# Optimization experiments

Hardware: AMD Instinct MI355X
Metric: run time of the kernel (lower is better)

Reference implementation:

```python
import jax, jax.numpy as jnp
import numpy as np

NUM_HEADS = 16
SQ, B, E = 2048, 4, 1024
SKV = 2049  # 1 text token + SQ motion tokens


def setup_inputs() -> dict:
    key = jax.random.key(0)
    ks = jax.random.split(key, 12)
    s = 1.0 / np.sqrt(E)
    inp = {
        "q": jax.random.normal(ks[0], (SQ, B, E), jnp.float32),
        "kv": jax.random.normal(ks[1], (SKV, B, E), jnp.float32),
        "cond_positions_mask": jax.random.bernoulli(ks[2], 0.3, (B, SQ)),
        "Wq": jax.random.uniform(ks[3], (E, E), jnp.float32, -s, s),
        "bq": jnp.zeros((E,), jnp.float32),
        "Wk": jax.random.uniform(ks[4], (E, E), jnp.float32, -s, s),
        "bk": jnp.zeros((E,), jnp.float32),
        "Wv": jax.random.uniform(ks[5], (E, E), jnp.float32, -s, s),
        "bv": jnp.zeros((E,), jnp.float32),
        "Wo": jax.random.uniform(ks[6], (E, E), jnp.float32, -s, s),
        "bo": jnp.zeros((E,), jnp.float32),
    }
    return inp


def _dual_causal_mask(cond_positions_mask, seq_len_q, seq_len_kv):
    # returns (B, Sq, Skv) bool, True = masked out
    motion_len = seq_len_kv - 1
    i = jnp.arange(seq_len_q)[:, None]
    j = jnp.arange(motion_len)[None, :]
    causal = (i < j)[None]                                  # (1, Sq, ml)
    ci = cond_positions_mask[:, :, None]                    # (B, Sq, 1)
    cj = cond_positions_mask[:, None, :motion_len]          # (B, 1, ml)
    cond_to_cond = ci & cj
    cond_to_gen = ci & ~cj
    motion_mask = (causal & ~cond_to_cond) | cond_to_gen    # (B, Sq, ml)
    b = cond_positions_mask.shape[0]
    text_col = jnp.zeros((b, seq_len_q, 1), bool)           # text token always visible
    return jnp.concatenate([text_col, motion_mask], axis=-1)


def reference(q, kv, cond_positions_mask, Wq, bq, Wk, bk, Wv, bv, Wo, bo):
    seq_len_q, batch, embed_dim = q.shape
    seq_len_kv = kv.shape[0]
    head_dim = embed_dim // NUM_HEADS
    qb = q.transpose(1, 0, 2)   # (B, Sq, E)
    kvb = kv.transpose(1, 0, 2)  # (B, Skv, E)
    Q = (qb @ Wq.T + bq).reshape(batch, seq_len_q, NUM_HEADS, head_dim)
    K = (kvb @ Wk.T + bk).reshape(batch, seq_len_kv, NUM_HEADS, head_dim)
    V = (kvb @ Wv.T + bv).reshape(batch, seq_len_kv, NUM_HEADS, head_dim)
    scores = jnp.einsum("bqhd,bkhd->bhqk", Q, K) / np.sqrt(head_dim).astype(np.float32)
    mask = _dual_causal_mask(cond_positions_mask, seq_len_q, seq_len_kv)
    scores = jnp.where(mask[:, None], -jnp.inf, scores)
    attn = jax.nn.softmax(scores, axis=-1)                  # (B, H, Sq, Skv)
    out = jnp.einsum("bhqk,bkhd->bqhd", attn, V).reshape(batch, seq_len_q, embed_dim)
    out = out @ Wo.T + bo
    return out.transpose(1, 0, 2), attn.mean(axis=1)
```

## Files before the change

### kernel.cpp

```cpp
#include <hip/hip_runtime.h>
#include <hip/hip_bf16.h>

#define B_ 4
#define H_ 16
#define D_ 64
#define E_ 1024
#define SQ_ 2048
#define SKV_ 2049
#define SKVP_ 2080
#define QSCALE 0.18033688011112042f

typedef __attribute__((ext_vector_type(8))) short short8;
typedef __attribute__((ext_vector_type(4))) float f32x4;
typedef __attribute__((ext_vector_type(16))) float f32x16;
typedef __attribute__((ext_vector_type(4))) unsigned int u32x4;
typedef __attribute__((ext_vector_type(4))) float float4v;

static __device__ __forceinline__ float ex2(float x) {
    return __builtin_amdgcn_exp2f(x);
}

static __device__ __forceinline__ unsigned short f2bf(float f) {
    unsigned int u = __float_as_uint(f);
    u += 0x7FFFu + ((u >> 16) & 1u);
    return (unsigned short)(u >> 16);
}
static __device__ __forceinline__ unsigned int pack2(float a, float b) {
    union { __hip_bfloat162 h; unsigned int u; } cv;
    cv.h = __float22bfloat162_rn(make_float2(a, b));
    return cv.u;
}

static __device__ __forceinline__ f32x4 mfma16(short8 a, short8 b, f32x4 c) {
    return __builtin_amdgcn_mfma_f32_16x16x32_bf16(a, b, c, 0, 0, 0);
}
static __device__ __forceinline__ f32x16 mfma32(short8 a, short8 b, f32x16 c) {
    return __builtin_amdgcn_mfma_f32_32x32x16_bf16(a, b, c, 0, 0, 0);
}

__global__ void cvt_bf16_kernel(const float* __restrict__ in,
                                unsigned short* __restrict__ out, int n8) {
    for (int i = blockIdx.x * blockDim.x + threadIdx.x; i < n8; i += gridDim.x * blockDim.x) {
        const float4v a = *(const float4v*)&in[(size_t)i * 8];
        const float4v b = *(const float4v*)&in[(size_t)i * 8 + 4];
        u32x4 o;
        o[0] = pack2(a[0], a[1]);
        o[1] = pack2(a[2], a[3]);
        o[2] = pack2(b[0], b[1]);
        o[3] = pack2(b[2], b[3]);
        *(u32x4*)&out[(size_t)i * 8] = o;
    }
}

__global__ void decode_mask_kernel(const void* __restrict__ mraw,
                                   unsigned char* __restrict__ condm) {
    __shared__ int flags[2];
    const int t = threadIdx.x;
    if (t < 2) flags[t] = 1;
    __syncthreads();
    const unsigned int* wp = (const unsigned int*)mraw;
    int okI = 1, okF = 1;
    for (int i = t; i < 2048; i += 256) {
        unsigned int w = wp[i];
        if (w > 1u) okI = 0;
        if (w != 0u && w != 0x3F800000u) okF = 0;
    }
    if (!okI) atomicAnd(&flags[0], 0);
    if (!okF) atomicAnd(&flags[1], 0);
    __syncthreads();
    const int isWord = flags[0] | flags[1];
    for (int i = t; i < B_ * SQ_; i += 256) {
        unsigned char v;
        if (isWord) v = (unsigned char)(wp[i] != 0u);
        else        v = (unsigned char)(((const unsigned char*)mraw)[i] != 0);
        condm[i] = v;
    }
}

template <int MODE>
__global__ __launch_bounds__(256, 2)
void gemm128_kernel(const unsigned short* __restrict__ Abf,
                    const unsigned short* __restrict__ Wbf,
                    const float* __restrict__ bias, void* __restrict__ Outp,
                    int nrows, int nrb) {
    const int bid = blockIdx.x;
    const int xcd = bid & 7;
    const int pos = bid >> 3;
    const int cb = pos & 7;
    const int rb = (pos >> 3) * 8 + xcd;
    if (rb >= nrb) return;
    const int row0 = rb * 128, col0 = cb * 128;

    __shared__ unsigned short As[128][40];
    __shared__ unsigned short Ws[128][40];
    const int t = threadIdx.x;
    const int w = t >> 6, lane = t & 63;
    const int wm = w >> 1, wn = w & 1;
    const int lr = lane & 15, lg = lane >> 4, lk = lg * 8;
    const int srow = t >> 1, sc0 = (t & 1) * 16;
    int ar = row0 + srow;
    if (ar >= nrows) ar = nrows - 1;
    const int wrow = col0 + srow;

    f32x4 acc[4][4] = {};

#pragma unroll 1
    for (int k0 = 0; k0 < E_; k0 += 32) {
        {
            const unsigned short* ap = &Abf[(size_t)ar * E_ + k0 + sc0];
            *(short8*)&As[srow][sc0] = *(const short8*)&ap[0];
            *(short8*)&As[srow][sc0 + 8] = *(const short8*)&ap[8];
        }
        {
            const unsigned short* wp2 = &Wbf[(size_t)wrow * E_ + k0 + sc0];
            *(short8*)&Ws[srow][sc0] = *(const short8*)&wp2[0];
            *(short8*)&Ws[srow][sc0 + 8] = *(const short8*)&wp2[8];
        }
        __syncthreads();
        short8 af[4], bf[4];
#pragma unroll
        for (int mi = 0; mi < 4; ++mi) af[mi] = *(const short8*)&As[wm * 64 + mi * 16 + lr][lk];
#pragma unroll
        for (int ni = 0; ni < 4; ++ni) bf[ni] = *(const short8*)&Ws[wn * 64 + ni * 16 + lr][lk];
#pragma unroll
        for (int mi = 0; mi < 4; ++mi)
#pragma unroll
            for (int ni = 0; ni < 4; ++ni)
                acc[mi][ni] = mfma16(af[mi], bf[ni], acc[mi][ni]);
        __syncthreads();
    }

#pragma unroll
    for (int ni = 0; ni < 4; ++ni) {
        const int c = col0 + wn * 64 + ni * 16 + lr;
        const float bv = bias[c];
        const int h = c >> 6, d = c & 63;
#pragma unroll
        for (int mi = 0; mi < 4; ++mi) {
#pragma unroll
            for (int r4 = 0; r4 < 4; ++r4) {
                const int r = row0 + wm * 64 + mi * 16 + lg * 4 + r4;
                if (r >= nrows) continue;
                float v = acc[mi][ni][r4] + bv;
                if constexpr (MODE == 0) {
                    v *= QSCALE;
                    const int sq = r >> 2, b = r & 3;
                    ((unsigned short*)Outp)[(((size_t)(b * H_ + h) * SQ_) + sq) * D_ + d] = f2bf(v);
                } else if constexpr (MODE == 1) {
                    const int kvi = r >> 2, b = r & 3;
                    ((unsigned short*)Outp)[(((size_t)(b * H_ + h) * SKVP_) + kvi) * D_ + d] = f2bf(v);
                } else if constexpr (MODE == 2) {
                    const int kvi = r >> 2, b = r & 3;
                    ((unsigned short*)Outp)[(((size_t)(b * H_ + h) * D_) + d) * SKVP_ + kvi] = f2bf(v);
                } else {
                    ((float*)Outp)[(size_t)r * E_ + c] = v;
                }
            }
        }
    }
}

__global__ void zero_pad_kernel(unsigned short* __restrict__ Kb,
                                unsigned short* __restrict__ Vt) {
    const int idx = blockIdx.x * blockDim.x + threadIdx.x;
    const int NK = 64 * 31 * 64;
    if (idx < NK) {
        const int bh = idx / (31 * 64);
        const int rem = idx - bh * 31 * 64;
        const int kvi = SKV_ + rem / 64;
        const int d = rem & 63;
        Kb[((size_t)bh * SKVP_ + kvi) * D_ + d] = 0;
    } else {
        const int j = idx - NK;
        if (j < 4096 * 31) {
            const int row = j / 31;
            const int kvi = SKV_ + (j - row * 31);
            Vt[(size_t)row * SKVP_ + kvi] = 0;
        }
    }
}

__global__ __launch_bounds__(256, 4)
void attn_fwd_kernel(const unsigned short* __restrict__ Qb, const unsigned short* __restrict__ Kb,
                     const unsigned short* __restrict__ Vt, const unsigned char* __restrict__ condm,
                     unsigned short* __restrict__ OP, float* __restrict__ Mst,
                     float* __restrict__ Lst) {
    const int h = blockIdx.y, b = blockIdx.z;
    const int bh = b * H_ + h;
    const int t = threadIdx.x, w = t >> 6, lane = t & 63;
    const int ql = lane & 31;
    const int hi = lane >> 5;
    const int qg = blockIdx.x * 128 + w * 32 + ql;

    __shared__ unsigned short Ks[64 * 64];
    __shared__ unsigned short Vs[64][72];
    __shared__ unsigned int cjb[66];

    for (int g = t; g < 66; g += 256) {
        unsigned int wbits = 0;
        const int base = g * 32;
#pragma unroll 4
        for (int i = 0; i < 32; ++i) {
            const int kv = base + i;
            if (kv >= 1 && kv < SKV_) wbits |= ((unsigned int)condm[b * SQ_ + kv - 1]) << i;
        }
        cjb[g] = wbits;
    }

    const size_t qoff = ((size_t)bh * SQ_ + qg) * D_;
    short8 qf[4];
#pragma unroll
    for (int tt = 0; tt < 4; ++tt) qf[tt] = *(const short8*)&Qb[qoff + tt * 16 + hi * 8];

    const unsigned int ci = condm[b * SQ_ + qg];

    float m = -__builtin_inff(), l = 0.f;
    f32x16 o0 = {}, o1 = {};

    const int krow = t >> 2, kseg2 = (t & 3) * 2;
    const int vrow = t >> 2, vc0 = (t & 3) * 16;
    const unsigned short* Kbase = &Kb[(size_t)bh * SKVP_ * D_];
    const unsigned short* Vbase = &Vt[(size_t)bh * D_ * SKVP_];

#pragma unroll 1
    for (int kv0 = 0; kv0 < SKVP_; kv0 += 64) {
        __syncthreads();
        {
            int krg = kv0 + krow;
            if (krg > SKVP_ - 1) krg = SKVP_ - 1;
            const unsigned short* kp = &Kbase[(size_t)krg * D_];
            *(short8*)&Ks[krow * 64 + ((kseg2 ^ (krow & 7)) * 8)] = *(const short8*)&kp[kseg2 * 8];
            *(short8*)&Ks[krow * 64 + (((kseg2 + 1) ^ (krow & 7)) * 8)] = *(const short8*)&kp[(kseg2 + 1) * 8];
            int vc = kv0 + vc0;
            if (vc > SKVP_ - 8) vc = SKVP_ - 8;
            int vc2 = kv0 + vc0 + 8;
            if (vc2 > SKVP_ - 8) vc2 = SKVP_ - 8;
            const unsigned short* vp = &Vbase[(size_t)vrow * SKVP_];
            *(short8*)&Vs[vrow][vc0] = *(const short8*)&vp[vc];
            *(short8*)&Vs[vrow][vc0 + 8] = *(const short8*)&vp[vc2];
        }
        __syncthreads();

#pragma unroll
        for (int ksub = 0; ksub < 2; ++ksub) {
            const int kvg = kv0 + ksub * 32;
            f32x16 S = {};
#pragma unroll
            for (int tt = 0; tt < 4; ++tt) {
                const short8 kf = *(const short8*)&Ks[(ksub * 32 + ql) * 64 + (((2 * tt + hi) ^ (ql & 7)) * 8)];
                S = mfma32(kf, qf[tt], S);
            }

            const unsigned int cjw = cjb[kvg >> 5];
            const int T = qg + 1 - kvg;
            unsigned int causalw;
            if (T < 0) causalw = ~0u;
            else if (T >= 31) causalw = 0u;
            else causalw = (~0u) << (T + 1);
            unsigned int mb = ci ? ~cjw : causalw;
            if (kvg == 0) mb &= ~1u;
            const unsigned int mbs = mb >> (hi * 4);

#pragma unroll
            for (int r = 0; r < 16; ++r) {
                const int kc = (r & 3) + 8 * (r >> 2);
                S[r] = ((mbs >> kc) & 1u) ? -__builtin_inff() : S[r];
            }
            float t0 = fmaxf(fmaxf(S[0], S[1]), S[2]);
            float t1 = fmaxf(fmaxf(S[3], S[4]), S[5]);
            float t2 = fmaxf(fmaxf(S[6], S[7]), S[8]);
            float t3 = fmaxf(fmaxf(S[9], S[10]), S[11]);
            float t4 = fmaxf(fmaxf(S[12], S[13]), S[14]);
            float rmax = fmaxf(fmaxf(fmaxf(t0, t1), t2), fmaxf(fmaxf(t3, t4), S[15]));
            rmax = fmaxf(rmax, __shfl_xor(rmax, 32));

            if (!__all(rmax <= m + 8.0f)) {
                const float mn = fmaxf(m, rmax);
                const float alpha = ex2(m - mn);
                l *= alpha;
                o0 *= alpha;
                o1 *= alpha;
                m = mn;
            }

#pragma unroll
            for (int r = 0; r < 16; ++r) S[r] = ex2(S[r] - m);
            const float a0s = (S[0] + S[1]) + (S[2] + S[3]);
            const float a1s = (S[4] + S[5]) + (S[6] + S[7]);
            const float a2s = (S[8] + S[9]) + (S[10] + S[11]);
            const float a3s = (S[12] + S[13]) + (S[14] + S[15]);
            float psum = (a0s + a1s) + (a2s + a3s);
            psum += __shfl_xor(psum, 32);
            l += psum;

            const unsigned int w0 = pack2(S[0], S[1]);
            const unsigned int w1 = pack2(S[2], S[3]);
            const unsigned int w2 = pack2(S[4], S[5]);
            const unsigned int w3 = pack2(S[6], S[7]);
            const unsigned int w4 = pack2(S[8], S[9]);
            const unsigned int w5 = pack2(S[10], S[11]);
            const unsigned int w6 = pack2(S[12], S[13]);
            const unsigned int w7 = pack2(S[14], S[15]);
            const unsigned int x0 = __shfl_xor(w0, 32);
            const unsigned int x1 = __shfl_xor(w1, 32);
            const unsigned int x2 = __shfl_xor(w2, 32);
            const unsigned int x3 = __shfl_xor(w3, 32);
            const unsigned int x4 = __shfl_xor(w4, 32);
            const unsigned int x5 = __shfl_xor(w5, 32);
            const unsigned int x6 = __shfl_xor(w6, 32);
            const unsigned int x7 = __shfl_xor(w7, 32);
            union { u32x4 u; short8 s8; } pb0, pb1;
            pb0.u = (u32x4){hi ? x2 : w0, hi ? x3 : w1, hi ? w2 : x0, hi ? w3 : x1};
            pb1.u = (u32x4){hi ? x6 : w4, hi ? x7 : w5, hi ? w6 : x4, hi ? w7 : x5};

            const short8 vf00 = *(const short8*)&Vs[ql][ksub * 32 + hi * 8];
            const short8 vf01 = *(const short8*)&Vs[ql][ksub * 32 + 16 + hi * 8];
            const short8 vf10 = *(const short8*)&Vs[32 + ql][ksub * 32 + hi * 8];
            const short8 vf11 = *(const short8*)&Vs[32 + ql][ksub * 32 + 16 + hi * 8];
            o0 = mfma32(vf00, pb0.s8, o0);
            o0 = mfma32(vf01, pb1.s8, o0);
            o1 = mfma32(vf10, pb0.s8, o1);
            o1 = mfma32(vf11, pb1.s8, o1);
        }
    }

    const float linv = 1.0f / l;
    unsigned short* opbase = &OP[((size_t)qg * B_ + b) * E_ + h * D_];
#pragma unroll
    for (int rp = 0; rp < 8; ++rp) {
        const int r0 = rp * 2, r1 = r0 + 1;
        const int d = ((r0 & 3) + 8 * (r0 >> 2)) + 4 * hi;
        *(unsigned int*)(opbase + d) = pack2(o0[r0] * linv, o0[r1] * linv);
        *(unsigned int*)(opbase + 32 + d) = pack2(o1[r0] * linv, o1[r1] * linv);
    }
    if (hi == 0) {
        Mst[(size_t)bh * SQ_ + qg] = m;
        Lst[(size_t)bh * SQ_ + qg] = linv;
    }
}

__global__ __launch_bounds__(256, 4)
void attn_probs_kernel(const unsigned short* __restrict__ Qb, const unsigned short* __restrict__ Kb,
                       const float* __restrict__ Mst, const float* __restrict__ Linv,
                       const unsigned char* __restrict__ condm, float* __restrict__ out1) {
    const int kv0 = blockIdx.x * 64;
    const int b = blockIdx.z;
    const int t = threadIdx.x, w = t >> 6, lane = t & 63;
    const int ql = lane & 31, hi = lane >> 5;
    const int kc = w >> 1, qc = w & 1;
    const int qg = blockIdx.y * 64 + qc * 32 + ql;

    __shared__ char smem[17408];
    unsigned short* Ks = (unsigned short*)smem;
    float* Tr = (float*)smem;
    __shared__ unsigned int cjw2[2];

    if (t < 64) {
        const int kvv = kv0 + t;
        int pred = 0;
        if (kvv >= 1 && kvv < SKV_) pred = condm[b * SQ_ + kvv - 1];
        const unsigned long long bal = __ballot(pred != 0);
        if (t == 0) { cjw2[0] = (unsigned int)bal; cjw2[1] = (unsigned int)(bal >> 32); }
    }
    const unsigned int ci = condm[b * SQ_ + qg];
    __syncthreads();

    const int kvg = kv0 + kc * 32;
    unsigned int mb;
    {
        const unsigned int cjw = cjw2[kc];
        const int T = qg + 1 - kvg;
        unsigned int causalw;
        if (T < 0) causalw = ~0u;
        else if (T >= 31) causalw = 0u;
        else causalw = (~0u) << (T + 1);
        mb = ci ? ~cjw : causalw;
        if (kvg == 0) mb &= ~1u;
    }
    const unsigned int mbs = mb >> (hi * 4);

    const int krow = t >> 2;
    const int kseg2 = (t & 3) * 2;
    int ksrc = kv0 + krow;
    if (ksrc >= SKVP_) ksrc = SKVP_ - 1;

    float acc[16] = {};

#pragma unroll 1
    for (int h = 0; h < H_; ++h) {
        const int bh = b * H_ + h;
        __syncthreads();
        {
            const unsigned short* kp = &Kb[((size_t)bh * SKVP_ + ksrc) * D_];
            *(short8*)&Ks[krow * 64 + ((kseg2 ^ (krow & 7)) * 8)] = *(const short8*)&kp[kseg2 * 8];
            *(short8*)&Ks[krow * 64 + (((kseg2 + 1) ^ (krow & 7)) * 8)] = *(const short8*)&kp[(kseg2 + 1) * 8];
        }
        __syncthreads();

        const size_t qoff = ((size_t)bh * SQ_ + qg) * D_;
        short8 qf[4];
#pragma unroll
        for (int tt = 0; tt < 4; ++tt) qf[tt] = *(const short8*)&Qb[qoff + tt * 16 + hi * 8];
        const float mh = Mst[(size_t)bh * SQ_ + qg];
        const float li = Linv[(size_t)bh * SQ_ + qg] * (1.0f / 16.0f);

        f32x16 S = {};
#pragma unroll
        for (int tt = 0; tt < 4; ++tt) {
            const short8 kf = *(const short8*)&Ks[(kc * 32 + ql) * 64 + (((2 * tt + hi) ^ (ql & 7)) * 8)];
            S = mfma32(kf, qf[tt], S);
        }
#pragma unroll
        for (int r = 0; r < 16; ++r) {
            const int kk = (r & 3) + 8 * (r >> 2);
            const float p = ((mbs >> kk) & 1u) ? 0.f : ex2(S[r] - mh);
            acc[r] += p * li;
        }
    }

    __syncthreads();

    float* Trw = &Tr[w * (32 * 33)];
#pragma unroll
    for (int r = 0; r < 16; ++r) {
        const int kk = (r & 3) + 8 * (r >> 2) + 4 * hi;
        Trw[ql * 33 + kk] = acc[r];
    }
    const int kcol = kv0 + kc * 32 + ql;
    const int qb_w = blockIdx.y * 64 + qc * 32;
    if (kcol < SKV_) {
#pragma unroll
        for (int step = 0; step < 16; ++step) {
            const int q2 = step * 2 + hi;
            out1[((size_t)b * SQ_ + qb_w + q2) * SKV_ + kcol] = Trw[q2 * 33 + ql];
        }
    }
}

extern "C" void kernel_launch(void* const* d_in, const int* in_sizes, int n_in,
                              void* d_out, int out_size, void* d_ws, size_t ws_size,
                              hipStream_t stream) {
    const float* q   = (const float*)d_in[0];
    const float* kv  = (const float*)d_in[1];
    const void*  msk = d_in[2];
    const float* Wq  = (const float*)d_in[3];
    const float* bq  = (const float*)d_in[4];
    const float* Wk  = (const float*)d_in[5];
    const float* bk  = (const float*)d_in[6];
    const float* Wv  = (const float*)d_in[7];
    const float* bv  = (const float*)d_in[8];
    const float* Wo  = (const float*)d_in[9];
    const float* bo  = (const float*)d_in[10];

    char* ws = (char*)d_ws;
    unsigned short* qbf = (unsigned short*)(ws);
    unsigned short* OP  = (unsigned short*)(ws);
    unsigned short* kvbf= (unsigned short*)(ws + 16777216);
    unsigned short* Wqb = (unsigned short*)(ws + 33562624);
    unsigned short* Wkb = (unsigned short*)(ws + 35659776);
    unsigned short* Wvb = (unsigned short*)(ws + 37756928);
    unsigned short* Wob = (unsigned short*)(ws + 39854080);
    unsigned short* Qb  = (unsigned short*)(ws + 41951232);
    unsigned short* Kb  = (unsigned short*)(ws + 58728448);
    unsigned short* Vt  = (unsigned short*)(ws + 75767808);
    float*          Mst = (float*)(ws + 92807168);
    float*          Lst = (float*)(ws + 93331456);
    unsigned char* condm = (unsigned char*)(ws + 93855744);

    float* out0 = (float*)d_out;
    float* out1 = out0 + (size_t)SQ_ * B_ * E_;

    decode_mask_kernel<<<1, 256, 0, stream>>>(msk, condm);
    cvt_bf16_kernel<<<2048, 256, 0, stream>>>(q, qbf, (SQ_ * B_ * E_) / 8);
    cvt_bf16_kernel<<<2048, 256, 0, stream>>>(kv, kvbf, (SKV_ * B_ * E_) / 8);
    cvt_bf16_kernel<<<512, 256, 0, stream>>>(Wq, Wqb, (E_ * E_) / 8);
    cvt_bf16_kernel<<<512, 256, 0, stream>>>(Wk, Wkb, (E_ * E_) / 8);
    cvt_bf16_kernel<<<512, 256, 0, stream>>>(Wv, Wvb, (E_ * E_) / 8);
    cvt_bf16_kernel<<<512, 256, 0, stream>>>(Wo, Wob, (E_ * E_) / 8);
    gemm128_kernel<0><<<512, 256, 0, stream>>>(qbf, Wqb, bq, (void*)Qb, SQ_ * B_, 64);
    gemm128_kernel<1><<<576, 256, 0, stream>>>(kvbf, Wkb, bk, (void*)Kb, SKV_ * B_, 65);
    gemm128_kernel<2><<<576, 256, 0, stream>>>(kvbf, Wvb, bv, (void*)Vt, SKV_ * B_, 65);
    zero_pad_kernel<<<992, 256, 0, stream>>>(Kb, Vt);
    attn_fwd_kernel<<<dim3(16, 16, 4), 256, 0, stream>>>(Qb, Kb, Vt, condm, OP, Mst, Lst);
    attn_probs_kernel<<<dim3(33, 32, 4), 256, 0, stream>>>(Qb, Kb, Mst, Lst, condm, out1);
    gemm128_kernel<3><<<512, 256, 0, stream>>>(OP, Wob, bo, (void*)out0, SQ_ * B_, 64);
}
```

Before: 517.5 us.

## Double-buffer K/V tiles in attention kernels and remap probs blocks per XCD

```diff
diff --git a/kernel.cpp b/kernel.cpp
--- a/kernel.cpp
+++ b/kernel.cpp
@@ -192,8 +192,8 @@
     const int hi = lane >> 5;
     const int qg = blockIdx.x * 128 + w * 32 + ql;
 
-    __shared__ unsigned short Ks[64 * 64];
-    __shared__ unsigned short Vs[64][72];
+    __shared__ unsigned short Ks[2 * 64 * 64];
+    __shared__ unsigned short Vs[2][64][72];
     __shared__ unsigned int cjb[66];
 
     for (int g = t; g < 66; g += 256) {
@@ -222,32 +222,49 @@
     const unsigned short* Kbase = &Kb[(size_t)bh * SKVP_ * D_];
     const unsigned short* Vbase = &Vt[(size_t)bh * D_ * SKVP_];
 
+    {
+        const unsigned short* kp = &Kbase[(size_t)krow * D_];
+        const short8 k0 = *(const short8*)&kp[kseg2 * 8];
+        const short8 k1 = *(const short8*)&kp[(kseg2 + 1) * 8];
+        const unsigned short* vp = &Vbase[(size_t)vrow * SKVP_];
+        const short8 v0 = *(const short8*)&vp[vc0];
+        const short8 v1 = *(const short8*)&vp[vc0 + 8];
+        *(short8*)&Ks[krow * 64 + ((kseg2 ^ (krow & 7)) * 8)] = k0;
+        *(short8*)&Ks[krow * 64 + (((kseg2 + 1) ^ (krow & 7)) * 8)] = k1;
+        *(short8*)&Vs[0][vrow][vc0] = v0;
+        *(short8*)&Vs[0][vrow][vc0 + 8] = v1;
+    }
+    __syncthreads();
+
 #pragma unroll 1
-    for (int kv0 = 0; kv0 < SKVP_; kv0 += 64) {
-        __syncthreads();
-        {
-            int krg = kv0 + krow;
+    for (int it = 0; it < 33; ++it) {
+        const int buf = it & 1;
+        const int kv0 = it * 64;
+        short8 nk0, nk1, nv0, nv1;
+        if (it < 32) {
+            const int kvn = kv0 + 64;
+            int krg = kvn + krow;
             if (krg > SKVP_ - 1) krg = SKVP_ - 1;
             const unsigned short* kp = &Kbase[(size_t)krg * D_];
-            *(short8*)&Ks[krow * 64 + ((kseg2 ^ (krow & 7)) * 8)] = *(const short8*)&kp[kseg2 * 8];
-            *(short8*)&Ks[krow * 64 + (((kseg2 + 1) ^ (krow & 7)) * 8)] = *(const short8*)&kp[(kseg2 + 1) * 8];
-            int vc = kv0 + vc0;
+            nk0 = *(const short8*)&kp[kseg2 * 8];
+            nk1 = *(const short8*)&kp[(kseg2 + 1) * 8];
+            int vc = kvn + vc0;
             if (vc > SKVP_ - 8) vc = SKVP_ - 8;
-            int vc2 = kv0 + vc0 + 8;
+            int vc2 = kvn + vc0 + 8;
             if (vc2 > SKVP_ - 8) vc2 = SKVP_ - 8;
             const unsigned short* vp = &Vbase[(size_t)vrow * SKVP_];
-            *(short8*)&Vs[vrow][vc0] = *(const short8*)&vp[vc];
-            *(short8*)&Vs[vrow][vc0 + 8] = *(const short8*)&vp[vc2];
-        }
-        __syncthreads();
-
+            nv0 = *(const short8*)&vp[vc];
+            nv1 = *(const short8*)&vp[vc2];
+        }
+
+        const unsigned short* Ksb = &Ks[buf * 4096];
 #pragma unroll
         for (int ksub = 0; ksub < 2; ++ksub) {
             const int kvg = kv0 + ksub * 32;
             f32x16 S = {};
 #pragma unroll
             for (int tt = 0; tt < 4; ++tt) {
-                const short8 kf = *(const short8*)&Ks[(ksub * 32 + ql) * 64 + (((2 * tt + hi) ^ (ql & 7)) * 8)];
+                const short8 kf = *(const short8*)&Ksb[(ksub * 32 + ql) * 64 + (((2 * tt + hi) ^ (ql & 7)) * 8)];
                 S = mfma32(kf, qf[tt], S);
             }
 
@@ -313,15 +330,24 @@
             pb0.u = (u32x4){hi ? x2 : w0, hi ? x3 : w1, hi ? w2 : x0, hi ? w3 : x1};
             pb1.u = (u32x4){hi ? x6 : w4, hi ? x7 : w5, hi ? w6 : x4, hi ? w7 : x5};
 
-            const short8 vf00 = *(const short8*)&Vs[ql][ksub * 32 + hi * 8];
-            const short8 vf01 = *(const short8*)&Vs[ql][ksub * 32 + 16 + hi * 8];
-            const short8 vf10 = *(const short8*)&Vs[32 + ql][ksub * 32 + hi * 8];
-            const short8 vf11 = *(const short8*)&Vs[32 + ql][ksub * 32 + 16 + hi * 8];
+            const short8 vf00 = *(const short8*)&Vs[buf][ql][ksub * 32 + hi * 8];
+            const short8 vf01 = *(const short8*)&Vs[buf][ql][ksub * 32 + 16 + hi * 8];
+            const short8 vf10 = *(const short8*)&Vs[buf][32 + ql][ksub * 32 + hi * 8];
+            const short8 vf11 = *(const short8*)&Vs[buf][32 + ql][ksub * 32 + 16 + hi * 8];
             o0 = mfma32(vf00, pb0.s8, o0);
             o0 = mfma32(vf01, pb1.s8, o0);
             o1 = mfma32(vf10, pb0.s8, o1);
             o1 = mfma32(vf11, pb1.s8, o1);
         }
+
+        if (it < 32) {
+            const int nb = (buf ^ 1) * 4096;
+            *(short8*)&Ks[nb + krow * 64 + ((kseg2 ^ (krow & 7)) * 8)] = nk0;
+            *(short8*)&Ks[nb + krow * 64 + (((kseg2 + 1) ^ (krow & 7)) * 8)] = nk1;
+            *(short8*)&Vs[buf ^ 1][vrow][vc0] = nv0;
+            *(short8*)&Vs[buf ^ 1][vrow][vc0 + 8] = nv1;
+        }
+        __syncthreads();
     }
 
     const float linv = 1.0f / l;
@@ -343,12 +369,20 @@
 void attn_probs_kernel(const unsigned short* __restrict__ Qb, const unsigned short* __restrict__ Kb,
                        const float* __restrict__ Mst, const float* __restrict__ Linv,
                        const unsigned char* __restrict__ condm, float* __restrict__ out1) {
-    const int kv0 = blockIdx.x * 64;
-    const int b = blockIdx.z;
+    const int bid = blockIdx.x;
+    const int xcd = bid & 7;
+    const int pos = bid >> 3;
+    const int qi = pos & 3;
+    const int rest = pos >> 2;
+    const int kvb = rest % 33;
+    const int b = rest / 33;
+    const int qblk = xcd * 4 + qi;
+    const int kv0 = kvb * 64;
+
     const int t = threadIdx.x, w = t >> 6, lane = t & 63;
     const int ql = lane & 31, hi = lane >> 5;
     const int kc = w >> 1, qc = w & 1;
-    const int qg = blockIdx.y * 64 + qc * 32 + ql;
+    const int qg = qblk * 64 + qc * 32 + ql;
 
     __shared__ char smem[17408];
     unsigned short* Ks = (unsigned short*)smem;
@@ -363,6 +397,19 @@
         if (t == 0) { cjw2[0] = (unsigned int)bal; cjw2[1] = (unsigned int)(bal >> 32); }
     }
     const unsigned int ci = condm[b * SQ_ + qg];
+
+    const int krow = t >> 2;
+    const int kseg2 = (t & 3) * 2;
+    int ksrc = kv0 + krow;
+    if (ksrc >= SKVP_) ksrc = SKVP_ - 1;
+
+    {
+        const unsigned short* kp = &Kb[((size_t)(b * H_) * SKVP_ + ksrc) * D_];
+        const short8 k0 = *(const short8*)&kp[kseg2 * 8];
+        const short8 k1 = *(const short8*)&kp[(kseg2 + 1) * 8];
+        *(short8*)&Ks[krow * 64 + ((kseg2 ^ (krow & 7)) * 8)] = k0;
+        *(short8*)&Ks[krow * 64 + (((kseg2 + 1) ^ (krow & 7)) * 8)] = k1;
+    }
     __syncthreads();
 
     const int kvg = kv0 + kc * 32;
@@ -379,23 +426,18 @@
     }
     const unsigned int mbs = mb >> (hi * 4);
 
-    const int krow = t >> 2;
-    const int kseg2 = (t & 3) * 2;
-    int ksrc = kv0 + krow;
-    if (ksrc >= SKVP_) ksrc = SKVP_ - 1;
-
     float acc[16] = {};
 
 #pragma unroll 1
     for (int h = 0; h < H_; ++h) {
+        const int buf = h & 1;
         const int bh = b * H_ + h;
-        __syncthreads();
-        {
-            const unsigned short* kp = &Kb[((size_t)bh * SKVP_ + ksrc) * D_];
-            *(short8*)&Ks[krow * 64 + ((kseg2 ^ (krow & 7)) * 8)] = *(const short8*)&kp[kseg2 * 8];
-            *(short8*)&Ks[krow * 64 + (((kseg2 + 1) ^ (krow & 7)) * 8)] = *(const short8*)&kp[(kseg2 + 1) * 8];
-        }
-        __syncthreads();
+        short8 nk0, nk1;
+        if (h < H_ - 1) {
+            const unsigned short* kp = &Kb[((size_t)(bh + 1) * SKVP_ + ksrc) * D_];
+            nk0 = *(const short8*)&kp[kseg2 * 8];
+            nk1 = *(const short8*)&kp[(kseg2 + 1) * 8];
+        }
 
         const size_t qoff = ((size_t)bh * SQ_ + qg) * D_;
         short8 qf[4];
@@ -404,10 +446,11 @@
         const float mh = Mst[(size_t)bh * SQ_ + qg];
         const float li = Linv[(size_t)bh * SQ_ + qg] * (1.0f / 16.0f);
 
+        const unsigned short* Ksb = &Ks[buf * 4096];
         f32x16 S = {};
 #pragma unroll
         for (int tt = 0; tt < 4; ++tt) {
-            const short8 kf = *(const short8*)&Ks[(kc * 32 + ql) * 64 + (((2 * tt + hi) ^ (ql & 7)) * 8)];
+            const short8 kf = *(const short8*)&Ksb[(kc * 32 + ql) * 64 + (((2 * tt + hi) ^ (ql & 7)) * 8)];
             S = mfma32(kf, qf[tt], S);
         }
 #pragma unroll
@@ -416,9 +459,14 @@
             const float p = ((mbs >> kk) & 1u) ? 0.f : ex2(S[r] - mh);
             acc[r] += p * li;
         }
-    }
-
-    __syncthreads();
+
+        if (h < H_ - 1) {
+            const int nb = (buf ^ 1) * 4096;
+            *(short8*)&Ks[nb + krow * 64 + ((kseg2 ^ (krow & 7)) * 8)] = nk0;
+            *(short8*)&Ks[nb + krow * 64 + (((kseg2 + 1) ^ (krow & 7)) * 8)] = nk1;
+        }
+        __syncthreads();
+    }
 
     float* Trw = &Tr[w * (32 * 33)];
 #pragma unroll
@@ -427,7 +475,7 @@
         Trw[ql * 33 + kk] = acc[r];
     }
     const int kcol = kv0 + kc * 32 + ql;
-    const int qb_w = blockIdx.y * 64 + qc * 32;
+    const int qb_w = qblk * 64 + qc * 32;
     if (kcol < SKV_) {
 #pragma unroll
         for (int step = 0; step < 16; ++step) {
@@ -482,6 +530,6 @@
     gemm128_kernel<2><<<576, 256, 0, stream>>>(kvbf, Wvb, bv, (void*)Vt, SKV_ * B_, 65);
     zero_pad_kernel<<<992, 256, 0, stream>>>(Kb, Vt);
     attn_fwd_kernel<<<dim3(16, 16, 4), 256, 0, stream>>>(Qb, Kb, Vt, condm, OP, Mst, Lst);
-    attn_probs_kernel<<<dim3(33, 32, 4), 256, 0, stream>>>(Qb, Kb, Mst, Lst, condm, out1);
+    attn_probs_kernel<<<4224, 256, 0, stream>>>(Qb, Kb, Mst, Lst, condm, out1);
     gemm128_kernel<3><<<512, 256, 0, stream>>>(OP, Wob, bo, (void*)out0, SQ_ * B_, 64);
 }
```

Measured after the change: 511.0 us. About the same (-1.3%).
